# Optimization experiments

Measured on AMD Instinct MI355X. Metric: run time of the kernel, lower is better.

Reference implementation:

```python
import jax, jax.numpy as jnp
import numpy as np

EMBED = 2048
MLP = 8192
EPS = 1e-5


def setup_inputs() -> dict:
    key = jax.random.key(0)
    ks = jax.random.split(key, 16)
    s = 0.02
    inp = {
        "x": jax.random.normal(ks[0], (2, 2048, EMBED), dtype=jnp.float32),
        "wq": jax.random.normal(ks[1], (EMBED, EMBED), dtype=jnp.float32) * s,
        "bq": jnp.zeros((EMBED,), jnp.float32),
        "wk": jax.random.normal(ks[2], (EMBED, EMBED), dtype=jnp.float32) * s,
        "bk": jnp.zeros((EMBED,), jnp.float32),
        "wv": jax.random.normal(ks[3], (EMBED, EMBED), dtype=jnp.float32) * s,
        "bv": jnp.zeros((EMBED,), jnp.float32),
        "wd": jax.random.normal(ks[4], (EMBED, EMBED), dtype=jnp.float32) * s,
        "bd": jnp.zeros((EMBED,), jnp.float32),
        "ln_g": jnp.ones((EMBED,), jnp.float32),
        "ln_b": jnp.zeros((EMBED,), jnp.float32),
        "w1": jax.random.normal(ks[5], (MLP, EMBED), dtype=jnp.float32) * s,
        "b1": jnp.zeros((MLP,), jnp.float32),
        "w2": jax.random.normal(ks[6], (EMBED, MLP), dtype=jnp.float32) * s,
        "b2": jnp.zeros((EMBED,), jnp.float32),
    }
    return inp


def _layernorm(x, g, b):
    mu = jnp.mean(x, axis=-1, keepdims=True)
    var = jnp.mean(jnp.square(x - mu), axis=-1, keepdims=True)
    return (x - mu) * jax.lax.rsqrt(var + EPS) * g + b


def reference(x, wq, bq, wk, bk, wv, bv, wd, bd, ln_g, ln_b, w1, b1, w2, b2):
    # Single-head attention; scale uses full embed_dim (rotary_emb.dim == embed_dim).
    q = jnp.einsum("bse,fe->bsf", x, wq) + bq
    k = jnp.einsum("bse,fe->bsf", x, wk) + bk
    v = jnp.einsum("bse,fe->bsf", x, wv) + bv
    scores = jnp.einsum("bqe,bke->bqk", q, k) / jnp.sqrt(jnp.float32(EMBED))
    probs = jax.nn.softmax(scores, axis=-1)
    ctx = jnp.einsum("bqk,bke->bqe", probs, v)
    attn_out = jnp.einsum("bse,fe->bsf", ctx, wd) + bd
    # residual (dropout is identity in eval mode)
    h = x + attn_out
    h = _layernorm(h, ln_g, ln_b)
    mlp = jnp.einsum("bse,fe->bsf", h, w1) + b1
    mlp = jax.nn.gelu(mlp, approximate=False)
    mlp = jnp.einsum("bsf,ef->bse", mlp, w2) + b2
    return h + mlp
```

## Files before the change

### kernel.cpp

```cpp
#include <hip/hip_runtime.h>
#include <math.h>


#define SEQ 2048
#define EMB 2048
#define MLPD 8192

typedef __attribute__((ext_vector_type(8))) short short8;
typedef __attribute__((ext_vector_type(4))) float floatx4;
typedef unsigned short ushort;

__device__ __forceinline__ short f2bf(float f) {
  union { float f; unsigned u; } v; v.f = f;
  unsigned r = v.u + 0x7FFFu + ((v.u >> 16) & 1u);
  return (short)(r >> 16);
}

__device__ __forceinline__ void gload16(const ushort* g, ushort* l) {
  __builtin_amdgcn_global_load_lds(
      (__attribute__((address_space(1))) void*)g,
      (__attribute__((address_space(3))) void*)(unsigned)(unsigned long)l,
      16, 0, 0);
}

enum { EPI_QKV = 0, EPI_SCORES = 1, EPI_PV = 2, EPI_RES = 3, EPI_GELU = 4 };

template<int EPI>
__global__ __launch_bounds__(512, 2)
void gemm256(const ushort* __restrict__ A, const ushort* __restrict__ B,
             const float* __restrict__ bias, void* __restrict__ Cp,
             int N, int K, int lda, int ldb, int ldc,
             long sA, long sB, long sC, float scale)
{
  extern __shared__ ushort lds[];
  const int t = threadIdx.x;
  const int lane = t & 63, w = t >> 6;
  const int wm = w >> 2, wn = w & 3;
  const long bm = (long)blockIdx.y * 256;
  const long bn = (long)blockIdx.x * 256;
  A += (long)blockIdx.z * sA;
  B += (long)blockIdx.z * sB;

  const int srow = (w << 3) + (lane >> 3);
  const int gcol = (lane & 7) ^ ((lane >> 3) & 7);
  const ushort* Ab = A + (bm + srow) * (long)lda + gcol * 8;
  const ushort* Bb = B + (bn + srow) * (long)ldb + gcol * 8;
  ushort* lw = lds + (w << 9);

#define STG_A0(LOFF, KK) do { gload16(Ab + (KK), lw + (LOFF)); \
    gload16(Ab + 64L * lda + (KK), lw + (LOFF) + 4096); } while (0)
#define STG_A1(LOFF, KK) do { gload16(Ab + 128L * lda + (KK), lw + (LOFF)); \
    gload16(Ab + 192L * lda + (KK), lw + (LOFF) + 4096); } while (0)
#define STG_B0(LOFF, KK) do { gload16(Bb + (KK), lw + (LOFF)); \
    gload16(Bb + 64L * ldb + (KK), lw + (LOFF) + 4096); } while (0)
#define STG_B1(LOFF, KK) do { gload16(Bb + 128L * ldb + (KK), lw + (LOFF)); \
    gload16(Bb + 192L * ldb + (KK), lw + (LOFF) + 4096); } while (0)

  const int l15 = lane & 15, q = lane >> 4, swz = l15 & 7;
  const int kx0 = (q ^ swz) << 3;
  const int kx1 = ((4 + q) ^ swz) << 3;
  const int arow = (wm << 13) + l15 * 64;
  const int brow = 16384 + ((wn >> 1) << 13) + ((wn & 1) << 12) + l15 * 64;

  floatx4 acc[8][4];
#pragma unroll
  for (int m = 0; m < 8; ++m)
#pragma unroll
    for (int n = 0; n < 4; ++n) acc[m][n] = (floatx4)0.0f;

  short8 A0[8], A1[8], B0[4], B1[4];

#define LDS8(IDX) (*(const short8*)&lds[IDX])
#define BARR() __builtin_amdgcn_s_barrier()

#define KTILE(CB, KS) do {                                                \
                                                        \
    _Pragma("unroll") for (int mf = 0; mf < 8; ++mf)                      \
      A0[mf] = LDS8((CB) + arow + mf * 1024 + kx0);                       \
    _Pragma("unroll") for (int nf = 0; nf < 4; ++nf)                      \
      B0[nf] = LDS8((CB) + brow + nf * 1024 + kx0);                       \
    _Pragma("unroll") for (int mf = 0; mf < 8; ++mf)                      \
      A1[mf] = LDS8((CB) + arow + mf * 1024 + kx1);                       \
    __builtin_amdgcn_s_setprio(1);                                        \
    _Pragma("unroll") for (int mf = 0; mf < 8; ++mf)                      \
      _Pragma("unroll") for (int nf = 0; nf < 4; ++nf)                    \
        acc[mf][nf] = __builtin_amdgcn_mfma_f32_16x16x32_bf16(            \
            A0[mf], B0[nf], acc[mf][nf], 0, 0, 0);                        \
    __builtin_amdgcn_s_setprio(0);                                        \
    _Pragma("unroll") for (int nf = 0; nf < 4; ++nf)                      \
      B1[nf] = LDS8((CB) + brow + nf * 1024 + kx1);                       \
    asm volatile("s_waitcnt lgkmcnt(0)" ::: "memory");                    \
    BARR();                                                               \
    \
    STG_A0((CB) + 0, KS);     STG_A1((CB) + 8192, KS);                    \
    STG_B0((CB) + 16384, KS); STG_B1((CB) + 24576, KS);                   \
    __builtin_amdgcn_s_setprio(1);                                        \
    _Pragma("unroll") for (int mf = 0; mf < 8; ++mf)                      \
      _Pragma("unroll") for (int nf = 0; nf < 4; ++nf)                    \
        acc[mf][nf] = __builtin_amdgcn_mfma_f32_16x16x32_bf16(            \
            A1[mf], B1[nf], acc[mf][nf], 0, 0, 0);                        \
    __builtin_amdgcn_s_setprio(0);                                        \
    asm volatile("s_waitcnt vmcnt(8)" ::: "memory");                      \
    BARR();                                                               \
  } while (0)

  STG_A0(0, 0);              STG_A1(8192, 0);
  STG_B0(16384, 0);          STG_B1(24576, 0);
  {
    const int k1p = (K > 64) ? 64 : 0;
    STG_A0(32768 + 0, k1p);     STG_A1(32768 + 8192, k1p);
    STG_B0(32768 + 16384, k1p); STG_B1(32768 + 24576, k1p);
  }
  asm volatile("s_waitcnt vmcnt(8)" ::: "memory");
  BARR();

  const int NT = K >> 6;
  for (int kt = 0; kt < NT; kt += 2) {
    const int k2 = ((kt + 2 < NT) ? kt + 2 : NT - 1) << 6;
    const int k3 = ((kt + 3 < NT) ? kt + 3 : NT - 1) << 6;
    KTILE(0,     k2);
    KTILE(32768, k3);
  }
  asm volatile("s_waitcnt vmcnt(0)" ::: "memory");
#undef KTILE
#undef LDS8
#undef STG_A0
#undef STG_A1
#undef STG_B0
#undef STG_B1

  const int lq = lane >> 4;
#pragma unroll
  for (int mf = 0; mf < 8; ++mf) {
#pragma unroll
    for (int nf = 0; nf < 4; ++nf) {
#pragma unroll
      for (int i = 0; i < 4; ++i) {
        const long r = bm + wm * 128 + mf * 16 + lq * 4 + i;
        const long c = bn + wn * 64 + nf * 16 + l15;
        float val = acc[mf][nf][i];
        if constexpr (EPI == EPI_QKV) {
          val += bias[c];
          ((ushort*)Cp)[r * (long)ldc + c] = (ushort)f2bf(val);
        } else if constexpr (EPI == EPI_SCORES) {
          ((float*)Cp)[(long)blockIdx.z * sC + r * (long)ldc + c] = val * scale;
        } else {
          val += bias[c];
          float g = 0.5f * val * (1.0f + erff(val * 0.70710678118f));
          ((ushort*)Cp)[r * (long)ldc + c] = (ushort)f2bf(g);
        }
      }
    }
  }
}

template<int EPI>
__global__ __launch_bounds__(256)
void gemm_bt(const ushort* __restrict__ A, const ushort* __restrict__ B,
             const float* __restrict__ bias, const float* __restrict__ res,
             void* __restrict__ Cp, int N, int K,
             int lda, int ldb, int ldc,
             long sA, long sB, long sC, float scale)
{
  __shared__ ushort As[128 * 32];
  __shared__ ushort Bs[128 * 32];

  const int t = threadIdx.x;
  const int lane = t & 63, wid = t >> 6;
  const int wm = wid >> 1, wn = wid & 1;
  const long bm = (long)blockIdx.y * 128;
  const long bn = (long)blockIdx.x * 128;
  A += (long)blockIdx.z * sA;
  B += (long)blockIdx.z * sB;

  const int srow = (wid << 5) + (lane >> 2);
  const int scol = (lane & 3) << 3;
  const ushort* a0 = A + (bm + srow) * (long)lda + scol;
  const ushort* a1 = a0 + 16L * lda;
  const ushort* b0 = B + (bn + srow) * (long)ldb + scol;
  const ushort* b1 = b0 + 16L * ldb;
  ushort* lA0 = As + (wid << 10);
  ushort* lA1 = lA0 + 512;
  ushort* lB0 = Bs + (wid << 10);
  ushort* lB1 = lB0 + 512;

  floatx4 acc[4][4];
#pragma unroll
  for (int m = 0; m < 4; ++m)
#pragma unroll
    for (int n = 0; n < 4; ++n) acc[m][n] = (floatx4)0.0f;

  const int l15 = lane & 15, kq = (lane >> 4) << 3;
  const int abase = ((wm << 6) + l15) * 32 + kq;
  const int bbase = ((wn << 6) + l15) * 32 + kq;

  for (int kb = 0; kb < K; kb += 32) {
    gload16(a0 + kb, lA0);
    gload16(a1 + kb, lA1);
    gload16(b0 + kb, lB0);
    gload16(b1 + kb, lB1);
    __syncthreads();

    short8 a[4], b[4];
#pragma unroll
    for (int m = 0; m < 4; ++m)
      a[m] = *reinterpret_cast<const short8*>(&As[abase + m * (16 * 32)]);
#pragma unroll
    for (int n = 0; n < 4; ++n)
      b[n] = *reinterpret_cast<const short8*>(&Bs[bbase + n * (16 * 32)]);
#pragma unroll
    for (int m = 0; m < 4; ++m)
#pragma unroll
      for (int n = 0; n < 4; ++n)
        acc[m][n] = __builtin_amdgcn_mfma_f32_16x16x32_bf16(a[m], b[n], acc[m][n], 0, 0, 0);
    __syncthreads();
  }

  const int lq = lane >> 4;
#pragma unroll
  for (int m = 0; m < 4; ++m) {
#pragma unroll
    for (int n = 0; n < 4; ++n) {
#pragma unroll
      for (int i = 0; i < 4; ++i) {
        const long r = bm + wm * 64 + m * 16 + lq * 4 + i;
        const long c = bn + wn * 64 + n * 16 + l15;
        float val = acc[m][n][i];
        if constexpr (EPI == EPI_SCORES) {
          ((float*)Cp)[(long)blockIdx.z * sC + r * (long)ldc + c] = val * scale;
        } else if constexpr (EPI == EPI_PV) {
          ((ushort*)Cp)[(long)blockIdx.z * sC + r * (long)ldc + c] = (ushort)f2bf(val);
        }
      }
    }
  }
}

__global__ __launch_bounds__(256)
void reduce2(const float* __restrict__ p0, const float* __restrict__ p1,
             const float* __restrict__ bias, const float* __restrict__ res,
             float* __restrict__ out)
{
  const long i = ((long)blockIdx.x * 256 + threadIdx.x) * 8;
  const int c = (int)(i & 2047);
  float4 a0 = *(const float4*)(p0 + i),  a1 = *(const float4*)(p0 + i + 4);
  float4 q0 = *(const float4*)(p1 + i),  q1 = *(const float4*)(p1 + i + 4);
  float4 r0 = *(const float4*)(res + i), r1 = *(const float4*)(res + i + 4);
  float4 b0 = *(const float4*)(bias + c), b1 = *(const float4*)(bias + c + 4);
  float4 o0 = {a0.x + q0.x + r0.x + b0.x, a0.y + q0.y + r0.y + b0.y,
               a0.z + q0.z + r0.z + b0.z, a0.w + q0.w + r0.w + b0.w};
  float4 o1 = {a1.x + q1.x + r1.x + b1.x, a1.y + q1.y + r1.y + b1.y,
               a1.z + q1.z + r1.z + b1.z, a1.w + q1.w + r1.w + b1.w};
  *(float4*)(out + i) = o0;
  *(float4*)(out + i + 4) = o1;
}

__global__ __launch_bounds__(256)
void cvt8(const float* __restrict__ s, ushort* __restrict__ d) {
  const long i = ((long)blockIdx.x * 256 + threadIdx.x) * 8;
  float4 a = *reinterpret_cast<const float4*>(s + i);
  float4 b = *reinterpret_cast<const float4*>(s + i + 4);
  short8 v;
  v[0] = f2bf(a.x); v[1] = f2bf(a.y); v[2] = f2bf(a.z); v[3] = f2bf(a.w);
  v[4] = f2bf(b.x); v[5] = f2bf(b.y); v[6] = f2bf(b.z); v[7] = f2bf(b.w);
  *reinterpret_cast<short8*>(d + i) = v;
}

__global__ __launch_bounds__(256)
void concat3(const float* __restrict__ b0, const float* __restrict__ b1,
             const float* __restrict__ b2, float* __restrict__ dst) {
  const int i = blockIdx.x * 256 + threadIdx.x;
  dst[i] = (i < 2048) ? b0[i] : (i < 4096) ? b1[i - 2048] : b2[i - 4096];
}

__global__ __launch_bounds__(256)
void transpose_v(const ushort* __restrict__ qkv, ushort* __restrict__ vT) {
  __shared__ ushort tile[32][33];
  const int b = blockIdx.z;
  const int s0 = blockIdx.x * 32, e0 = blockIdx.y * 32;
  const int tx = threadIdx.x & 31, ty = threadIdx.x >> 5;
#pragma unroll
  for (int i = 0; i < 4; ++i) {
    const long s = (long)b * SEQ + s0 + ty + i * 8;
    tile[ty + i * 8][tx] = qkv[s * 6144 + 4096 + e0 + tx];
  }
  __syncthreads();
#pragma unroll
  for (int i = 0; i < 4; ++i) {
    const long e = (long)b * SEQ + e0 + ty + i * 8;
    vT[e * SEQ + s0 + tx] = tile[tx][ty + i * 8];
  }
}

__global__ __launch_bounds__(256)
void softmax_rows(const float* __restrict__ S, ushort* __restrict__ P) {
  const long row = blockIdx.x;
  const float* src = S + row * 2048;
  const int t = threadIdx.x, lane = t & 63, wid = t >> 6;
  float4 a = *reinterpret_cast<const float4*>(src + t * 8);
  float4 b = *reinterpret_cast<const float4*>(src + t * 8 + 4);
  float v[8] = {a.x, a.y, a.z, a.w, b.x, b.y, b.z, b.w};
  float m = v[0];
#pragma unroll
  for (int i = 1; i < 8; ++i) m = fmaxf(m, v[i]);
#pragma unroll
  for (int o = 32; o; o >>= 1) m = fmaxf(m, __shfl_xor(m, o));
  __shared__ float rm[4], rs[4];
  if (!lane) rm[wid] = m;
  __syncthreads();
  m = fmaxf(fmaxf(rm[0], rm[1]), fmaxf(rm[2], rm[3]));
  float e[8], s = 0.f;
#pragma unroll
  for (int i = 0; i < 8; ++i) { e[i] = __expf(v[i] - m); s += e[i]; }
#pragma unroll
  for (int o = 32; o; o >>= 1) s += __shfl_xor(s, o);
  if (!lane) rs[wid] = s;
  __syncthreads();
  s = rs[0] + rs[1] + rs[2] + rs[3];
  const float inv = 1.0f / s;
  short8 wv;
#pragma unroll
  for (int i = 0; i < 8; ++i) wv[i] = f2bf(e[i] * inv);
  *reinterpret_cast<short8*>(P + row * 2048 + t * 8) = wv;
}

__global__ __launch_bounds__(256)
void layernorm_fused(const float* __restrict__ p0, const float* __restrict__ p1,
                     const float* __restrict__ bias, const float* __restrict__ res,
                     const float* __restrict__ g, const float* __restrict__ bb,
                     float* __restrict__ H, ushort* __restrict__ Hb) {
  const long row = blockIdx.x;
  const long base = row * 2048;
  const int t = threadIdx.x, lane = t & 63, wid = t >> 6;
  const long i = base + t * 8;
  const int c0 = t * 8;
  float v[8];
  {
    float4 a0 = *(const float4*)(p0 + i),  a1 = *(const float4*)(p0 + i + 4);
    float4 q0 = *(const float4*)(p1 + i),  q1 = *(const float4*)(p1 + i + 4);
    float4 r0 = *(const float4*)(res + i), r1 = *(const float4*)(res + i + 4);
    float4 b0 = *(const float4*)(bias + c0), b1 = *(const float4*)(bias + c0 + 4);
    v[0] = a0.x + q0.x + r0.x + b0.x; v[1] = a0.y + q0.y + r0.y + b0.y;
    v[2] = a0.z + q0.z + r0.z + b0.z; v[3] = a0.w + q0.w + r0.w + b0.w;
    v[4] = a1.x + q1.x + r1.x + b1.x; v[5] = a1.y + q1.y + r1.y + b1.y;
    v[6] = a1.z + q1.z + r1.z + b1.z; v[7] = a1.w + q1.w + r1.w + b1.w;
  }
  float s = 0.f, ss = 0.f;
#pragma unroll
  for (int i2 = 0; i2 < 8; ++i2) { s += v[i2]; ss += v[i2] * v[i2]; }
#pragma unroll
  for (int o = 32; o; o >>= 1) { s += __shfl_xor(s, o); ss += __shfl_xor(ss, o); }
  __shared__ float r1s[4], r2s[4];
  if (!lane) { r1s[wid] = s; r2s[wid] = ss; }
  __syncthreads();
  s = r1s[0] + r1s[1] + r1s[2] + r1s[3];
  ss = r2s[0] + r2s[1] + r2s[2] + r2s[3];
  const float mu = s * (1.0f / 2048.0f);
  const float var = ss * (1.0f / 2048.0f) - mu * mu;
  const float inv = rsqrtf(var + 1e-5f);
  float o0[8];
  short8 wv;
#pragma unroll
  for (int i2 = 0; i2 < 8; ++i2) {
    const int c = c0 + i2;
    o0[i2] = (v[i2] - mu) * inv * g[c] + bb[c];
    wv[i2] = f2bf(o0[i2]);
  }
  float4 w0 = {o0[0], o0[1], o0[2], o0[3]}, w1 = {o0[4], o0[5], o0[6], o0[7]};
  *reinterpret_cast<float4*>(H + i) = w0;
  *reinterpret_cast<float4*>(H + i + 4) = w1;
  *reinterpret_cast<short8*>(Hb + i) = wv;
}

extern "C" void kernel_launch(void* const* d_in, const int* in_sizes, int n_in,
                              void* d_out, int out_size, void* d_ws, size_t ws_size,
                              hipStream_t stream) {
  const float* x    = (const float*)d_in[0];
  const float* wq   = (const float*)d_in[1];
  const float* bq   = (const float*)d_in[2];
  const float* wk   = (const float*)d_in[3];
  const float* bk   = (const float*)d_in[4];
  const float* wv   = (const float*)d_in[5];
  const float* bv   = (const float*)d_in[6];
  const float* wd   = (const float*)d_in[7];
  const float* bd   = (const float*)d_in[8];
  const float* ln_g = (const float*)d_in[9];
  const float* ln_b = (const float*)d_in[10];
  const float* w1   = (const float*)d_in[11];
  const float* b1   = (const float*)d_in[12];
  const float* w2   = (const float*)d_in[13];
  const float* b2   = (const float*)d_in[14];
  float* out = (float*)d_out;

  (void)hipFuncSetAttribute((const void*)&gemm256<EPI_QKV>,
      hipFuncAttributeMaxDynamicSharedMemorySize, 131072);
  (void)hipFuncSetAttribute((const void*)&gemm256<EPI_GELU>,
      hipFuncAttributeMaxDynamicSharedMemorySize, 131072);
  (void)hipFuncSetAttribute((const void*)&gemm256<EPI_SCORES>,
      hipFuncAttributeMaxDynamicSharedMemorySize, 131072);

  char* p = (char*)d_ws;
  const size_t MB = 1048576;
  ushort* wdb    = (ushort*)(p + 0 * MB);
  ushort* w1b    = (ushort*)(p + 8 * MB);
  ushort* w2b    = (ushort*)(p + 40 * MB);
  float*  bqkv   = (float*) (p + 72 * MB);
  ushort* xb     = (ushort*)(p + 73 * MB);
  ushort* probs  = xb;
  ushort* qkv    = (ushort*)(p + 89 * MB);
  float*  partA  = (float*) (p + 89 * MB);
  ushort* mlpb   = (ushort*)(p + 89 * MB);
  ushort* vT     = (ushort*)(p + 137 * MB);
  ushort* wqkvb  = (ushort*)(p + 153 * MB);
  float*  scores = (float*) (p + 153 * MB);
  ushort* ctx    = (ushort*)(p + 153 * MB);
  float*  partM0 = (float*) (p + 0 * MB);
  float*  partM1 = (float*) (p + 153 * MB);
  float*  h      = (float*) (p + 185 * MB);
  ushort* hb     = (ushort*)(p + 217 * MB);

  const dim3 blk(256), blk512(512);
  const long SQ = (long)SEQ * SEQ;

  cvt8<<<4096, blk, 0, stream>>>(x, xb);
  cvt8<<<2048, blk, 0, stream>>>(wq, wqkvb);
  cvt8<<<2048, blk, 0, stream>>>(wk, wqkvb + 4194304);
  cvt8<<<2048, blk, 0, stream>>>(wv, wqkvb + 8388608);
  cvt8<<<2048, blk, 0, stream>>>(wd, wdb);
  cvt8<<<8192, blk, 0, stream>>>(w1, w1b);
  cvt8<<<8192, blk, 0, stream>>>(w2, w2b);
  concat3<<<24, blk, 0, stream>>>(bq, bk, bv, bqkv);

  gemm256<EPI_QKV><<<dim3(24, 16, 1), blk512, 131072, stream>>>(
      xb, wqkvb, bqkv, qkv, 6144, 2048, 2048, 2048, 6144, 0, 0, 0, 1.f);

  transpose_v<<<dim3(64, 64, 2), blk, 0, stream>>>(qkv, vT);

  gemm_bt<EPI_SCORES><<<dim3(16, 16, 2), blk, 0, stream>>>(
      qkv, qkv + 2048, nullptr, nullptr, scores, 2048, 2048, 6144, 6144, 2048,
      2048L * 6144, 2048L * 6144, SQ, 0.022097086912079608f);

  softmax_rows<<<dim3(4096), blk, 0, stream>>>(scores, probs);

  gemm_bt<EPI_PV><<<dim3(16, 16, 2), blk, 0, stream>>>(
      probs, vT, nullptr, nullptr, ctx, 2048, 2048, 2048, 2048, 2048,
      SQ, SQ, SQ, 1.f);

  gemm256<EPI_SCORES><<<dim3(8, 16, 2), blk512, 131072, stream>>>(
      ctx, wdb, nullptr, partA, 2048, 1024, 2048, 2048, 2048,
      1024, 1024, 8388608, 1.f);

  layernorm_fused<<<4096, blk, 0, stream>>>(
      partA, partA + 8388608, bd, x, ln_g, ln_b, h, hb);

  gemm256<EPI_GELU><<<dim3(32, 16, 1), blk512, 131072, stream>>>(
      hb, w1b, b1, mlpb, 8192, 2048, 2048, 2048, 8192, 0, 0, 0, 1.f);

  gemm256<EPI_SCORES><<<dim3(8, 16, 2), blk512, 131072, stream>>>(
      mlpb, w2b, nullptr, partM0, 2048, 4096, 8192, 8192, 2048,
      4096, 4096, (long)(153 * MB / 4), 1.f);
  reduce2<<<4096, blk, 0, stream>>>(partM0, partM1, b2, h, out);
}
```

Measured before the change: 676.8 us.

## Replace 256x256 GEMM with 128x256 tile kernel and unify attention GEMMs

Replaces the 256x256-tile, K=64-step GEMM (128KB LDS, 2 blocks/CU) with a 128x256-tile, K=32-step kernel using 48KB LDS and launch bounds for 4 blocks per CU. The older 128x128 gemm_bt kernel used for scores and PV is removed, and those GEMMs now also run through the new double-buffered kernel with an added PV epilogue. The goal is higher occupancy, a finer grid for better CU load balance, and async LDS prefetch for the attention GEMMs. In exchange, per-block data reuse is lower and barriers are more frequent per unit of K, which may hurt the large MLP GEMMs.

```diff
diff --git a/kernel.cpp b/kernel.cpp
--- a/kernel.cpp
+++ b/kernel.cpp
@@ -16,18 +16,18 @@
   return (short)(r >> 16);
 }
 
-__device__ __forceinline__ void gload16(const ushort* g, ushort* l) {
+__device__ __forceinline__ void gload16(const ushort* g, const ushort* l) {
   __builtin_amdgcn_global_load_lds(
       (__attribute__((address_space(1))) void*)g,
       (__attribute__((address_space(3))) void*)(unsigned)(unsigned long)l,
       16, 0, 0);
 }
 
-enum { EPI_QKV = 0, EPI_SCORES = 1, EPI_PV = 2, EPI_RES = 3, EPI_GELU = 4 };
+enum { EPI_QKV = 0, EPI_SCORES = 1, EPI_PV = 2, EPI_GELU = 4 };
 
 template<int EPI>
-__global__ __launch_bounds__(512, 2)
-void gemm256(const ushort* __restrict__ A, const ushort* __restrict__ B,
+__global__ __launch_bounds__(512, 4)
+void gemm128(const ushort* __restrict__ A, const ushort* __restrict__ B,
              const float* __restrict__ bias, void* __restrict__ Cp,
              int N, int K, int lda, int ldb, int ldc,
              long sA, long sB, long sC, float scale)
@@ -36,107 +36,84 @@
   const int t = threadIdx.x;
   const int lane = t & 63, w = t >> 6;
   const int wm = w >> 2, wn = w & 3;
-  const long bm = (long)blockIdx.y * 256;
+  const long bm = (long)blockIdx.y * 128;
   const long bn = (long)blockIdx.x * 256;
   A += (long)blockIdx.z * sA;
   B += (long)blockIdx.z * sB;
 
-  const int srow = (w << 3) + (lane >> 3);
-  const int gcol = (lane & 7) ^ ((lane >> 3) & 7);
-  const ushort* Ab = A + (bm + srow) * (long)lda + gcol * 8;
-  const ushort* Bb = B + (bn + srow) * (long)ldb + gcol * 8;
-  ushort* lw = lds + (w << 9);
-
-#define STG_A0(LOFF, KK) do { gload16(Ab + (KK), lw + (LOFF)); \
-    gload16(Ab + 64L * lda + (KK), lw + (LOFF) + 4096); } while (0)
-#define STG_A1(LOFF, KK) do { gload16(Ab + 128L * lda + (KK), lw + (LOFF)); \
-    gload16(Ab + 192L * lda + (KK), lw + (LOFF) + 4096); } while (0)
-#define STG_B0(LOFF, KK) do { gload16(Bb + (KK), lw + (LOFF)); \
-    gload16(Bb + 64L * ldb + (KK), lw + (LOFF) + 4096); } while (0)
-#define STG_B1(LOFF, KK) do { gload16(Bb + 128L * ldb + (KK), lw + (LOFF)); \
-    gload16(Bb + 192L * ldb + (KK), lw + (LOFF) + 4096); } while (0)
-
-  const int l15 = lane & 15, q = lane >> 4, swz = l15 & 7;
-  const int kx0 = (q ^ swz) << 3;
-  const int kx1 = ((4 + q) ^ swz) << 3;
-  const int arow = (wm << 13) + l15 * 64;
-  const int brow = 16384 + ((wn >> 1) << 13) + ((wn & 1) << 12) + l15 * 64;
-
-  floatx4 acc[8][4];
-#pragma unroll
-  for (int m = 0; m < 8; ++m)
+  const int grow = (w << 4) + (lane >> 2);
+  const int gcol = (lane & 3) ^ ((lane >> 2) & 3);
+  const ushort* Ag  = A + (bm + grow) * (long)lda + gcol * 8;
+  const ushort* Bg  = B + (bn + grow) * (long)ldb + gcol * 8;
+  const ushort* Bg2 = B + (bn + 128 + grow) * (long)ldb + gcol * 8;
+  const int lwA  = (w << 9);
+  const int lwB  = 4096 + (w << 9);
+  const int lwB2 = 8192 + (w << 9);
+
+#define STG(CB, KK) do {                                     \
+    gload16(Ag  + (KK), lds + (CB) + lwA);                   \
+    gload16(Bg  + (KK), lds + (CB) + lwB);                   \
+    gload16(Bg2 + (KK), lds + (CB) + lwB2); } while (0)
+
+  const int l15 = lane & 15, q = lane >> 4;
+  const int kx = (q ^ (l15 & 3)) << 3;
+  const int ar = ((wm << 6) + l15) * 32 + kx;
+  const int br = 4096 + ((wn << 6) + l15) * 32 + kx;
+
+  floatx4 acc[4][4];
+#pragma unroll
+  for (int m = 0; m < 4; ++m)
 #pragma unroll
     for (int n = 0; n < 4; ++n) acc[m][n] = (floatx4)0.0f;
 
-  short8 A0[8], A1[8], B0[4], B1[4];
+  short8 a[4], b[4];
 
 #define LDS8(IDX) (*(const short8*)&lds[IDX])
 #define BARR() __builtin_amdgcn_s_barrier()
 
-#define KTILE(CB, KS) do {                                                \
-                                                        \
-    _Pragma("unroll") for (int mf = 0; mf < 8; ++mf)                      \
-      A0[mf] = LDS8((CB) + arow + mf * 1024 + kx0);                       \
+#define ITER(CB, KS) do {                                                 \
+    _Pragma("unroll") for (int mf = 0; mf < 4; ++mf)                      \
+      a[mf] = LDS8((CB) + ar + mf * 512);                                 \
     _Pragma("unroll") for (int nf = 0; nf < 4; ++nf)                      \
-      B0[nf] = LDS8((CB) + brow + nf * 1024 + kx0);                       \
-    _Pragma("unroll") for (int mf = 0; mf < 8; ++mf)                      \
-      A1[mf] = LDS8((CB) + arow + mf * 1024 + kx1);                       \
+      b[nf] = LDS8((CB) + br + nf * 512);                                 \
     __builtin_amdgcn_s_setprio(1);                                        \
-    _Pragma("unroll") for (int mf = 0; mf < 8; ++mf)                      \
+    _Pragma("unroll") for (int mf = 0; mf < 4; ++mf)                      \
       _Pragma("unroll") for (int nf = 0; nf < 4; ++nf)                    \
         acc[mf][nf] = __builtin_amdgcn_mfma_f32_16x16x32_bf16(            \
-            A0[mf], B0[nf], acc[mf][nf], 0, 0, 0);                        \
+            a[mf], b[nf], acc[mf][nf], 0, 0, 0);                          \
     __builtin_amdgcn_s_setprio(0);                                        \
-    _Pragma("unroll") for (int nf = 0; nf < 4; ++nf)                      \
-      B1[nf] = LDS8((CB) + brow + nf * 1024 + kx1);                       \
-    asm volatile("s_waitcnt lgkmcnt(0)" ::: "memory");                    \
     BARR();                                                               \
-    \
-    STG_A0((CB) + 0, KS);     STG_A1((CB) + 8192, KS);                    \
-    STG_B0((CB) + 16384, KS); STG_B1((CB) + 24576, KS);                   \
-    __builtin_amdgcn_s_setprio(1);                                        \
-    _Pragma("unroll") for (int mf = 0; mf < 8; ++mf)                      \
-      _Pragma("unroll") for (int nf = 0; nf < 4; ++nf)                    \
-        acc[mf][nf] = __builtin_amdgcn_mfma_f32_16x16x32_bf16(            \
-            A1[mf], B1[nf], acc[mf][nf], 0, 0, 0);                        \
-    __builtin_amdgcn_s_setprio(0);                                        \
-    asm volatile("s_waitcnt vmcnt(8)" ::: "memory");                      \
+    STG(CB, KS);                                                          \
+    asm volatile("s_waitcnt vmcnt(3)" ::: "memory");                      \
     BARR();                                                               \
   } while (0)
 
-  STG_A0(0, 0);              STG_A1(8192, 0);
-  STG_B0(16384, 0);          STG_B1(24576, 0);
-  {
-    const int k1p = (K > 64) ? 64 : 0;
-    STG_A0(32768 + 0, k1p);     STG_A1(32768 + 8192, k1p);
-    STG_B0(32768 + 16384, k1p); STG_B1(32768 + 24576, k1p);
-  }
-  asm volatile("s_waitcnt vmcnt(8)" ::: "memory");
+  const int NT = K >> 5;
+
+  STG(0, 0);
+  STG(12288, 32);
+  asm volatile("s_waitcnt vmcnt(3)" ::: "memory");
   BARR();
 
-  const int NT = K >> 6;
   for (int kt = 0; kt < NT; kt += 2) {
-    const int k2 = ((kt + 2 < NT) ? kt + 2 : NT - 1) << 6;
-    const int k3 = ((kt + 3 < NT) ? kt + 3 : NT - 1) << 6;
-    KTILE(0,     k2);
-    KTILE(32768, k3);
+    const int k2 = ((kt + 2 < NT) ? kt + 2 : NT - 1) << 5;
+    const int k3 = ((kt + 3 < NT) ? kt + 3 : NT - 1) << 5;
+    ITER(0,     k2);
+    ITER(12288, k3);
   }
   asm volatile("s_waitcnt vmcnt(0)" ::: "memory");
-#undef KTILE
+#undef ITER
 #undef LDS8
-#undef STG_A0
-#undef STG_A1
-#undef STG_B0
-#undef STG_B1
+#undef STG
 
   const int lq = lane >> 4;
 #pragma unroll
-  for (int mf = 0; mf < 8; ++mf) {
+  for (int mf = 0; mf < 4; ++mf) {
 #pragma unroll
     for (int nf = 0; nf < 4; ++nf) {
 #pragma unroll
       for (int i = 0; i < 4; ++i) {
-        const long r = bm + wm * 128 + mf * 16 + lq * 4 + i;
+        const long r = bm + wm * 64 + mf * 16 + lq * 4 + i;
         const long c = bn + wn * 64 + nf * 16 + l15;
         float val = acc[mf][nf][i];
         if constexpr (EPI == EPI_QKV) {
@@ -144,92 +121,12 @@
           ((ushort*)Cp)[r * (long)ldc + c] = (ushort)f2bf(val);
         } else if constexpr (EPI == EPI_SCORES) {
           ((float*)Cp)[(long)blockIdx.z * sC + r * (long)ldc + c] = val * scale;
+        } else if constexpr (EPI == EPI_PV) {
+          ((ushort*)Cp)[(long)blockIdx.z * sC + r * (long)ldc + c] = (ushort)f2bf(val);
         } else {
           val += bias[c];
           float g = 0.5f * val * (1.0f + erff(val * 0.70710678118f));
           ((ushort*)Cp)[r * (long)ldc + c] = (ushort)f2bf(g);
-        }
-      }
-    }
-  }
-}
-
-template<int EPI>
-__global__ __launch_bounds__(256)
-void gemm_bt(const ushort* __restrict__ A, const ushort* __restrict__ B,
-             const float* __restrict__ bias, const float* __restrict__ res,
-             void* __restrict__ Cp, int N, int K,
-             int lda, int ldb, int ldc,
-             long sA, long sB, long sC, float scale)
-{
-  __shared__ ushort As[128 * 32];
-  __shared__ ushort Bs[128 * 32];
-
-  const int t = threadIdx.x;
-  const int lane = t & 63, wid = t >> 6;
-  const int wm = wid >> 1, wn = wid & 1;
-  const long bm = (long)blockIdx.y * 128;
-  const long bn = (long)blockIdx.x * 128;
-  A += (long)blockIdx.z * sA;
-  B += (long)blockIdx.z * sB;
-
-  const int srow = (wid << 5) + (lane >> 2);
-  const int scol = (lane & 3) << 3;
-  const ushort* a0 = A + (bm + srow) * (long)lda + scol;
-  const ushort* a1 = a0 + 16L * lda;
-  const ushort* b0 = B + (bn + srow) * (long)ldb + scol;
-  const ushort* b1 = b0 + 16L * ldb;
-  ushort* lA0 = As + (wid << 10);
-  ushort* lA1 = lA0 + 512;
-  ushort* lB0 = Bs + (wid << 10);
-  ushort* lB1 = lB0 + 512;
-
-  floatx4 acc[4][4];
-#pragma unroll
-  for (int m = 0; m < 4; ++m)
-#pragma unroll
-    for (int n = 0; n < 4; ++n) acc[m][n] = (floatx4)0.0f;
-
-  const int l15 = lane & 15, kq = (lane >> 4) << 3;
-  const int abase = ((wm << 6) + l15) * 32 + kq;
-  const int bbase = ((wn << 6) + l15) * 32 + kq;
-
-  for (int kb = 0; kb < K; kb += 32) {
-    gload16(a0 + kb, lA0);
-    gload16(a1 + kb, lA1);
-    gload16(b0 + kb, lB0);
-    gload16(b1 + kb, lB1);
-    __syncthreads();
-
-    short8 a[4], b[4];
-#pragma unroll
-    for (int m = 0; m < 4; ++m)
-      a[m] = *reinterpret_cast<const short8*>(&As[abase + m * (16 * 32)]);
-#pragma unroll
-    for (int n = 0; n < 4; ++n)
-      b[n] = *reinterpret_cast<const short8*>(&Bs[bbase + n * (16 * 32)]);
-#pragma unroll
-    for (int m = 0; m < 4; ++m)
-#pragma unroll
-      for (int n = 0; n < 4; ++n)
-        acc[m][n] = __builtin_amdgcn_mfma_f32_16x16x32_bf16(a[m], b[n], acc[m][n], 0, 0, 0);
-    __syncthreads();
-  }
-
-  const int lq = lane >> 4;
-#pragma unroll
-  for (int m = 0; m < 4; ++m) {
-#pragma unroll
-    for (int n = 0; n < 4; ++n) {
-#pragma unroll
-      for (int i = 0; i < 4; ++i) {
-        const long r = bm + wm * 64 + m * 16 + lq * 4 + i;
-        const long c = bn + wn * 64 + n * 16 + l15;
-        float val = acc[m][n][i];
-        if constexpr (EPI == EPI_SCORES) {
-          ((float*)Cp)[(long)blockIdx.z * sC + r * (long)ldc + c] = val * scale;
-        } else if constexpr (EPI == EPI_PV) {
-          ((ushort*)Cp)[(long)blockIdx.z * sC + r * (long)ldc + c] = (ushort)f2bf(val);
         }
       }
     }
@@ -392,13 +289,6 @@
   const float* b2   = (const float*)d_in[14];
   float* out = (float*)d_out;
 
-  (void)hipFuncSetAttribute((const void*)&gemm256<EPI_QKV>,
-      hipFuncAttributeMaxDynamicSharedMemorySize, 131072);
-  (void)hipFuncSetAttribute((const void*)&gemm256<EPI_GELU>,
-      hipFuncAttributeMaxDynamicSharedMemorySize, 131072);
-  (void)hipFuncSetAttribute((const void*)&gemm256<EPI_SCORES>,
-      hipFuncAttributeMaxDynamicSharedMemorySize, 131072);
-
   char* p = (char*)d_ws;
   const size_t MB = 1048576;
   ushort* wdb    = (ushort*)(p + 0 * MB);
@@ -421,6 +311,7 @@
 
   const dim3 blk(256), blk512(512);
   const long SQ = (long)SEQ * SEQ;
+  const size_t LDSB = 49152;
 
   cvt8<<<4096, blk, 0, stream>>>(x, xb);
   cvt8<<<2048, blk, 0, stream>>>(wq, wqkvb);
@@ -431,32 +322,32 @@
   cvt8<<<8192, blk, 0, stream>>>(w2, w2b);
   concat3<<<24, blk, 0, stream>>>(bq, bk, bv, bqkv);
 
-  gemm256<EPI_QKV><<<dim3(24, 16, 1), blk512, 131072, stream>>>(
+  gemm128<EPI_QKV><<<dim3(24, 32, 1), blk512, LDSB, stream>>>(
       xb, wqkvb, bqkv, qkv, 6144, 2048, 2048, 2048, 6144, 0, 0, 0, 1.f);
 
   transpose_v<<<dim3(64, 64, 2), blk, 0, stream>>>(qkv, vT);
 
-  gemm_bt<EPI_SCORES><<<dim3(16, 16, 2), blk, 0, stream>>>(
-      qkv, qkv + 2048, nullptr, nullptr, scores, 2048, 2048, 6144, 6144, 2048,
+  gemm128<EPI_SCORES><<<dim3(8, 16, 2), blk512, LDSB, stream>>>(
+      qkv, qkv + 2048, nullptr, scores, 2048, 2048, 6144, 6144, 2048,
       2048L * 6144, 2048L * 6144, SQ, 0.022097086912079608f);
 
   softmax_rows<<<dim3(4096), blk, 0, stream>>>(scores, probs);
 
-  gemm_bt<EPI_PV><<<dim3(16, 16, 2), blk, 0, stream>>>(
-      probs, vT, nullptr, nullptr, ctx, 2048, 2048, 2048, 2048, 2048,
+  gemm128<EPI_PV><<<dim3(8, 16, 2), blk512, LDSB, stream>>>(
+      probs, vT, nullptr, ctx, 2048, 2048, 2048, 2048, 2048,
       SQ, SQ, SQ, 1.f);
 
-  gemm256<EPI_SCORES><<<dim3(8, 16, 2), blk512, 131072, stream>>>(
+  gemm128<EPI_SCORES><<<dim3(8, 32, 2), blk512, LDSB, stream>>>(
       ctx, wdb, nullptr, partA, 2048, 1024, 2048, 2048, 2048,
       1024, 1024, 8388608, 1.f);
 
   layernorm_fused<<<4096, blk, 0, stream>>>(
       partA, partA + 8388608, bd, x, ln_g, ln_b, h, hb);
 
-  gemm256<EPI_GELU><<<dim3(32, 16, 1), blk512, 131072, stream>>>(
+  gemm128<EPI_GELU><<<dim3(32, 32, 1), blk512, LDSB, stream>>>(
       hb, w1b, b1, mlpb, 8192, 2048, 2048, 2048, 8192, 0, 0, 0, 1.f);
 
-  gemm256<EPI_SCORES><<<dim3(8, 16, 2), blk512, 131072, stream>>>(
+  gemm128<EPI_SCORES><<<dim3(8, 32, 2), blk512, LDSB, stream>>>(
       mlpb, w2b, nullptr, partM0, 2048, 4096, 8192, 8192, 2048,
       4096, 4096, (long)(153 * MB / 4), 1.f);
   reduce2<<<4096, blk, 0, stream>>>(partM0, partM1, b2, h, out);
```

New measurement: 707.7 us. +4.6%, slower.
